# Kernel optimization log

Measured on AMD Instinct MI355X. Metric: run time of the kernel, lower is better.

Reference implementation:

```python
import jax, jax.numpy as jnp
import numpy as np

N = 50000      # nodes
E = 800000     # edges (avg degree 16)
DIM = 128      # in_dim == out_dim
H = 8          # num_heads
D = DIM // H   # per-head dim = 16


def layer_norm(x, g, b, eps=1e-5):
    m = x.mean(-1, keepdims=True)
    v = ((x - m) ** 2).mean(-1, keepdims=True)
    return (x - m) / jnp.sqrt(v + eps) * g + b


def setup_inputs() -> dict:
    key = jax.random.key(0)
    ks = jax.random.split(key, 16)
    w = 0.02
    return {
        "x": jax.random.normal(ks[0], (N, DIM), dtype=jnp.float32),
        "src": jax.random.randint(ks[1], (E,), 0, N),
        "dst": jax.random.randint(ks[2], (E,), 0, N),
        "Wq": jax.random.normal(ks[3], (DIM, DIM), dtype=jnp.float32) * w,
        "bq": jnp.zeros((DIM,), dtype=jnp.float32),
        "Wk": jax.random.normal(ks[4], (DIM, DIM), dtype=jnp.float32) * w,
        "bk": jnp.zeros((DIM,), dtype=jnp.float32),
        "Wv": jax.random.normal(ks[5], (DIM, DIM), dtype=jnp.float32) * w,
        "bv": jnp.zeros((DIM,), dtype=jnp.float32),
        "Wo": jax.random.normal(ks[6], (DIM, DIM), dtype=jnp.float32) * w,
        "bo": jnp.zeros((DIM,), dtype=jnp.float32),
        "ln1_g": jnp.ones((DIM,), dtype=jnp.float32),
        "ln1_b": jnp.zeros((DIM,), dtype=jnp.float32),
        "ln2_g": jnp.ones((DIM,), dtype=jnp.float32),
        "ln2_b": jnp.zeros((DIM,), dtype=jnp.float32),
    }


def reference(x, src, dst, Wq, bq, Wk, bk, Wv, bv, Wo, bo, ln1_g, ln1_b, ln2_g, ln2_b):
    # Q/K/V projections, split into heads: [N, H, D]
    Q = (x @ Wq + bq).reshape(N, H, D)
    K = (x @ Wk + bk).reshape(N, H, D)
    V = (x @ Wv + bv).reshape(N, H, D)

    # per-edge src_dot_dst: (K[src] * Q[dst]).sum(-1) -> [E, H, 1]
    score = (K[src] * Q[dst]).sum(-1, keepdims=True)
    # scaled_exp with clamp(-5, 5)
    score = jnp.exp(jnp.clip(score / np.sqrt(D).astype(np.float32), -5.0, 5.0))

    # scatter-sum of V[src] * score into dst nodes -> wV [N, H, D]
    wV = jax.ops.segment_sum(V[src] * score, dst, num_segments=N)
    # (the original also computes z = segment_sum(score) but never uses it)

    # residual + LayerNorm
    h = x + wV.reshape(N, DIM)
    h = layer_norm(h, ln1_g, ln1_b)

    # sublayer wrapper: h + relu(O(norm(h)))  (dropout=0)
    h = h + jax.nn.relu(layer_norm(h, ln2_g, ln2_b) @ Wo + bo)
    return h
```

## Files before the change

### kernel.cpp

```cpp
#include <hip/hip_runtime.h>
#include <hip/hip_bf16.h>

#define N_NODES 50000
#define N_EDGES 800000
#define DIM     128
#define CAP     96
#define PREP_BLOCKS 258
#define QKV_BLOCKS  1563

typedef __attribute__((ext_vector_type(8))) short bf16x8;
typedef __attribute__((ext_vector_type(4))) float f32x4;
typedef __fp16 f16;
typedef __attribute__((ext_vector_type(2))) __fp16 f16x2;

__device__ __forceinline__ unsigned short f2bf(float f) {
    union { float f; unsigned u; } c; c.f = f;
    unsigned r = c.u + 0x7fffu + ((c.u >> 16) & 1u);
    return (unsigned short)(r >> 16);
}
__device__ __forceinline__ float bfhi(unsigned int u) {
    union { unsigned int u; float f; } c; c.u = u & 0xffff0000u; return c.f;
}
__device__ __forceinline__ float bflo(unsigned int u) {
    union { unsigned int u; float f; } c; c.u = u << 16; return c.f;
}
__device__ __forceinline__ float bfs(unsigned short s) {
    union { unsigned int u; float f; } c; c.u = (unsigned)s << 16; return c.f;
}
__device__ __forceinline__ void unpack8(uint4 w, float* f) {
    f[0] = bflo(w.x); f[1] = bfhi(w.x);
    f[2] = bflo(w.y); f[3] = bfhi(w.y);
    f[4] = bflo(w.z); f[5] = bfhi(w.z);
    f[6] = bflo(w.w); f[7] = bfhi(w.w);
}

__global__ __launch_bounds__(256) void prep_kernel(
    const float* __restrict__ Wq, const float* __restrict__ Wk,
    const float* __restrict__ Wv, const float* __restrict__ Wo,
    const float* __restrict__ bq, const float* __restrict__ bk,
    const float* __restrict__ bv,
    unsigned short* __restrict__ WT, unsigned short* __restrict__ WoT,
    float* __restrict__ bqkv, int* __restrict__ counts)
{
    const int t = blockIdx.x * 256 + threadIdx.x;
    if (t < N_NODES) counts[(unsigned)t << 4] = 0;
    if (t < 384 * 128) {
        int j = t >> 7, k = t & 127;
        int which = j >> 7, jj = j & 127;
        const float* W = which == 0 ? Wq : which == 1 ? Wk : Wv;
        WT[t] = f2bf(W[k * 128 + jj]);
    } else if (t < 384 * 128 + 128 * 128) {
        int t2 = t - 384 * 128;
        int j = t2 >> 7, k = t2 & 127;
        WoT[t2] = f2bf(Wo[k * 128 + j]);
    } else if (t < 384 * 128 + 128 * 128 + 384) {
        int j = t - (384 * 128 + 128 * 128);
        bqkv[j] = j < 128 ? bq[j] : j < 256 ? bk[j - 128] : bv[j - 256];
    }
}

__global__ __launch_bounds__(256) void qkv_fill_kernel(
    const float* __restrict__ x, const unsigned short* __restrict__ WT,
    const float* __restrict__ bqkv,
    const int* __restrict__ src, const int* __restrict__ dst,
    int* __restrict__ counts, unsigned short* __restrict__ bucket,
    unsigned short* __restrict__ Q, unsigned char* __restrict__ K8,
    unsigned short* __restrict__ Vh )
{
    __shared__ union {
        unsigned short xs[32][136];
        unsigned short cs[32][384];
    } sh;

    const int b = blockIdx.x;

    if (b & 1) {
        const int e0 = (b >> 1) * 512 + threadIdx.x;
        int s0 = 0, d0 = 0, s1 = 0, d1 = 0;
        const bool v0 = e0 < N_EDGES;
        const bool v1 = e0 + 256 < N_EDGES;
        if (v0) { s0 = src[e0]; d0 = dst[e0]; }
        if (v1) { s1 = src[e0 + 256]; d1 = dst[e0 + 256]; }
        if (v0) {
            const int pos = atomicAdd(&counts[(unsigned)d0 << 4], 1);
            if (pos < CAP) bucket[(unsigned)d0 * CAP + pos] = (unsigned short)s0;
        }
        if (v1) {
            const int pos = atomicAdd(&counts[(unsigned)d1 << 4], 1);
            if (pos < CAP) bucket[(unsigned)d1 * CAP + pos] = (unsigned short)s1;
        }
        return;
    }

    const int w   = threadIdx.x >> 6;
    const int l   = threadIdx.x & 63;
    const int l15 = l & 15;
    const int lk  = l >> 4;
    const int n0  = (b >> 1) * 32;

    for (int idx = threadIdx.x; idx < 32 * 32; idx += 256) {
        const int row = idx >> 5, c4 = idx & 31;
        const int node = n0 + row;
        unsigned short s0 = 0, s1 = 0, s2 = 0, s3 = 0;
        if (node < N_NODES) {
            float4 f = ((const float4*)(x + (size_t)node * 128))[c4];
            s0 = f2bf(f.x); s1 = f2bf(f.y); s2 = f2bf(f.z); s3 = f2bf(f.w);
        }
        unsigned short* p = &sh.xs[row][c4 * 4];
        p[0] = s0; p[1] = s1; p[2] = s2; p[3] = s3;
    }
    __syncthreads();

    f32x4 acc[6][2];
#pragma unroll
    for (int t = 0; t < 6; ++t)
#pragma unroll
        for (int rg = 0; rg < 2; ++rg) acc[t][rg] = (f32x4){0.f, 0.f, 0.f, 0.f};

#pragma unroll
    for (int kk = 0; kk < 4; ++kk) {
        const int kb = kk * 32 + lk * 8;
        bf16x8 a[2];
#pragma unroll
        for (int rg = 0; rg < 2; ++rg)
            a[rg] = *(const bf16x8*)(&sh.xs[rg * 16 + l15][kb]);
#pragma unroll
        for (int t = 0; t < 6; ++t) {
            const int j0 = w * 96 + t * 16;
            bf16x8 bb = *(const bf16x8*)(WT + (size_t)(j0 + l15) * 128 + kb);
            acc[t][0] = __builtin_amdgcn_mfma_f32_16x16x32_bf16(a[0], bb, acc[t][0], 0, 0, 0);
            acc[t][1] = __builtin_amdgcn_mfma_f32_16x16x32_bf16(a[1], bb, acc[t][1], 0, 0, 0);
        }
    }
    __syncthreads();

#pragma unroll
    for (int t = 0; t < 6; ++t) {
        const int j = w * 96 + t * 16 + l15;
        const float bias = bqkv[j];
#pragma unroll
        for (int rg = 0; rg < 2; ++rg)
#pragma unroll
            for (int r = 0; r < 4; ++r)
                sh.cs[rg * 16 + lk * 4 + r][j] = f2bf(acc[t][rg][r] + bias);
    }
    __syncthreads();

    for (int idx = threadIdx.x; idx < 32 * 16; idx += 256) {
        const int row = idx >> 4, c8 = idx & 15;
        const int node = n0 + row;
        if (node < N_NODES)
            *(uint4*)(Q + (size_t)node * 128 + c8 * 8) =
                ((const uint4*)&sh.cs[row][0])[c8];
    }
    for (int idx = threadIdx.x; idx < 32 * 16; idx += 256) {
        const int row = idx >> 4, c8 = idx & 15;
        const int node = n0 + row;
        if (node < N_NODES) {
            const unsigned short* p = &sh.cs[row][128 + c8 * 8];
            int w0 = __builtin_amdgcn_cvt_pk_fp8_f32(bfs(p[0]), bfs(p[1]), 0, false);
            w0     = __builtin_amdgcn_cvt_pk_fp8_f32(bfs(p[2]), bfs(p[3]), w0, true);
            int w1 = __builtin_amdgcn_cvt_pk_fp8_f32(bfs(p[4]), bfs(p[5]), 0, false);
            w1     = __builtin_amdgcn_cvt_pk_fp8_f32(bfs(p[6]), bfs(p[7]), w1, true);
            *(uint2*)(K8 + (size_t)node * 128 + c8 * 8) =
                make_uint2((unsigned)w0, (unsigned)w1);
        }
    }
    for (int idx = threadIdx.x; idx < 32 * 16; idx += 256) {
        const int row = idx >> 4, c8 = idx & 15;
        const int node = n0 + row;
        if (node < N_NODES) {
            const unsigned short* p = &sh.cs[row][256 + c8 * 8];
            union { uint4 u; f16x2 h[4]; } vv;
            vv.h[0] = __builtin_amdgcn_cvt_pkrtz(bfs(p[0]), bfs(p[1]));
            vv.h[1] = __builtin_amdgcn_cvt_pkrtz(bfs(p[2]), bfs(p[3]));
            vv.h[2] = __builtin_amdgcn_cvt_pkrtz(bfs(p[4]), bfs(p[5]));
            vv.h[3] = __builtin_amdgcn_cvt_pkrtz(bfs(p[6]), bfs(p[7]));
            *(uint4*)(Vh + (size_t)node * 128 + c8 * 8) = vv.u;
        }
    }
}

__device__ __forceinline__ void edge_accum(uint2 kw, uint4 vw,
                                           const float* q, f16x2* acc2)
{
    float kf[8];
#if __has_builtin(__builtin_amdgcn_cvt_pk_f32_fp8)
    {
        auto p0 = __builtin_amdgcn_cvt_pk_f32_fp8((int)kw.x, false);
        auto p1 = __builtin_amdgcn_cvt_pk_f32_fp8((int)kw.x, true);
        auto p2 = __builtin_amdgcn_cvt_pk_f32_fp8((int)kw.y, false);
        auto p3 = __builtin_amdgcn_cvt_pk_f32_fp8((int)kw.y, true);
        kf[0] = p0[0]; kf[1] = p0[1]; kf[2] = p1[0]; kf[3] = p1[1];
        kf[4] = p2[0]; kf[5] = p2[1]; kf[6] = p3[0]; kf[7] = p3[1];
    }
#else
    kf[0] = __builtin_amdgcn_cvt_f32_fp8(kw.x, 0);
    kf[1] = __builtin_amdgcn_cvt_f32_fp8(kw.x, 1);
    kf[2] = __builtin_amdgcn_cvt_f32_fp8(kw.x, 2);
    kf[3] = __builtin_amdgcn_cvt_f32_fp8(kw.x, 3);
    kf[4] = __builtin_amdgcn_cvt_f32_fp8(kw.y, 0);
    kf[5] = __builtin_amdgcn_cvt_f32_fp8(kw.y, 1);
    kf[6] = __builtin_amdgcn_cvt_f32_fp8(kw.y, 2);
    kf[7] = __builtin_amdgcn_cvt_f32_fp8(kw.y, 3);
#endif
    float dot = q[0]*kf[0] + q[1]*kf[1] + q[2]*kf[2] + q[3]*kf[3]
              + q[4]*kf[4] + q[5]*kf[5] + q[6]*kf[6] + q[7]*kf[7];
    dot += __shfl_xor(dot, 1);
    float z = fminf(fmaxf(dot * 0.25f, -5.f), 5.f);
    float sc = __expf(z);
    f16x2 sc2 = __builtin_amdgcn_cvt_pkrtz(sc, sc);
    union { uint4 u; f16x2 h[4]; } v; v.u = vw;
#pragma unroll
    for (int j = 0; j < 4; ++j)
        acc2[j] = __builtin_elementwise_fma(v.h[j], sc2, acc2[j]);
}

__global__ __launch_bounds__(256) void gather_ln_kernel(
    const float* __restrict__ x,
    const unsigned short* __restrict__ Qb, const unsigned char* __restrict__ K8,
    const unsigned short* __restrict__ Vh,
    const int* __restrict__ counts, const unsigned short* __restrict__ bucket,
    const float* __restrict__ g1, const float* __restrict__ b1,
    unsigned short* __restrict__ h )
{
    const int node = blockIdx.x * 4 + (threadIdx.x >> 6);
    if (node >= N_NODES) return;
    const unsigned lane = threadIdx.x & 15;
    const unsigned grp  = (threadIdx.x >> 4) & 3;

    const uint4* Q4 = (const uint4*)Qb;
    const uint2* K2 = (const uint2*)K8;
    const uint4* V4 = (const uint4*)Vh;

    const float4* x4 = (const float4*)(x + (size_t)node * DIM);
    const float4 xa = x4[lane * 2], xb = x4[lane * 2 + 1];

    float q[8];
    unpack8(Q4[(unsigned)node * 16u + lane], q);

    int cnt = counts[(unsigned)node << 4];
    if (cnt > CAP) cnt = CAP;
    const unsigned base = (unsigned)node * CAP;

    f16x2 acc2[4];
#pragma unroll
    for (int j = 0; j < 4; ++j) acc2[j] = (f16x2){(f16)0.f, (f16)0.f};

    int i = grp;
    for (; i + 4 < cnt; i += 8) {
        const unsigned s0 = bucket[base + i];
        const unsigned s1 = bucket[base + i + 4];
        const uint2 kw0 = K2[s0 * 16u + lane];
        const uint4 vw0 = V4[s0 * 16u + lane];
        const uint2 kw1 = K2[s1 * 16u + lane];
        const uint4 vw1 = V4[s1 * 16u + lane];
        edge_accum(kw0, vw0, q, acc2);
        edge_accum(kw1, vw1, q, acc2);
    }
    if (i < cnt) {
        const unsigned s0 = bucket[base + i];
        const uint2 kw0 = K2[s0 * 16u + lane];
        const uint4 vw0 = V4[s0 * 16u + lane];
        edge_accum(kw0, vw0, q, acc2);
    }

#pragma unroll
    for (int j = 0; j < 4; ++j) {
        float t = __builtin_bit_cast(float, acc2[j]);
        t = __shfl_xor(t, 16);
        acc2[j] += __builtin_bit_cast(f16x2, t);
        t = __builtin_bit_cast(float, acc2[j]);
        t = __shfl_xor(t, 32);
        acc2[j] += __builtin_bit_cast(f16x2, t);
    }
    float wv[8];
#pragma unroll
    for (int j = 0; j < 4; ++j) {
        wv[2 * j]     = (float)acc2[j][0];
        wv[2 * j + 1] = (float)acc2[j][1];
    }

    float a[8] = { xa.x + wv[0], xa.y + wv[1], xa.z + wv[2], xa.w + wv[3],
                   xb.x + wv[4], xb.y + wv[5], xb.z + wv[6], xb.w + wv[7] };

    float sum = 0.f;
#pragma unroll
    for (int j = 0; j < 8; ++j) sum += a[j];
#pragma unroll
    for (int m = 1; m < 16; m <<= 1) sum += __shfl_xor(sum, m);
    float mean = sum * (1.f / 128.f);
    float vs = 0.f;
#pragma unroll
    for (int j = 0; j < 8; ++j) { a[j] -= mean; vs += a[j] * a[j]; }
#pragma unroll
    for (int m = 1; m < 16; m <<= 1) vs += __shfl_xor(vs, m);
    float rstd = rsqrtf(vs * (1.f / 128.f) + 1e-5f);

    if ((threadIdx.x & 63) < 16) {
        const float4 g1a = ((const float4*)g1)[lane * 2], g1b = ((const float4*)g1)[lane * 2 + 1];
        const float4 b1a = ((const float4*)b1)[lane * 2], b1b = ((const float4*)b1)[lane * 2 + 1];
        float hv[8];
        hv[0] = a[0] * rstd * g1a.x + b1a.x;  hv[1] = a[1] * rstd * g1a.y + b1a.y;
        hv[2] = a[2] * rstd * g1a.z + b1a.z;  hv[3] = a[3] * rstd * g1a.w + b1a.w;
        hv[4] = a[4] * rstd * g1b.x + b1b.x;  hv[5] = a[5] * rstd * g1b.y + b1b.y;
        hv[6] = a[6] * rstd * g1b.z + b1b.z;  hv[7] = a[7] * rstd * g1b.w + b1b.w;

        uint4 up;
        up.x = (unsigned)f2bf(hv[0]) | ((unsigned)f2bf(hv[1]) << 16);
        up.y = (unsigned)f2bf(hv[2]) | ((unsigned)f2bf(hv[3]) << 16);
        up.z = (unsigned)f2bf(hv[4]) | ((unsigned)f2bf(hv[5]) << 16);
        up.w = (unsigned)f2bf(hv[6]) | ((unsigned)f2bf(hv[7]) << 16);
        ((uint4*)(h + (size_t)node * DIM))[lane] = up;
    }
}

__global__ __launch_bounds__(256) void out_mfma(
    const unsigned short* __restrict__ h, const unsigned short* __restrict__ WoT,
    const float* __restrict__ g2, const float* __restrict__ b2,
    const float* __restrict__ bo, float* __restrict__ out)
{
    __shared__ unsigned short hs[32][136];
    __shared__ union {
        unsigned short us[32][136];
        float ls[32][128];
    } shB;

    const int w   = threadIdx.x >> 6;
    const int l   = threadIdx.x & 63;
    const int l15 = l & 15;
    const int lk  = l >> 4;
    const int n0  = blockIdx.x * 32;

    for (int idx = threadIdx.x; idx < 32 * 16; idx += 256) {
        const int row = idx >> 4, c8 = idx & 15;
        const int node = n0 + row;
        uint4 v = make_uint4(0, 0, 0, 0);
        if (node < N_NODES)
            v = ((const uint4*)(h + (size_t)node * 128))[c8];
        *(uint4*)(&hs[row][c8 * 8]) = v;
    }
    __syncthreads();

    {
        const int row = threadIdx.x >> 3;
        const int sub = threadIdx.x & 7;
        float v[16];
#pragma unroll
        for (int j = 0; j < 16; ++j) v[j] = bfs(hs[row][sub * 16 + j]);
        float sum = 0.f;
#pragma unroll
        for (int j = 0; j < 16; ++j) sum += v[j];
#pragma unroll
        for (int m = 1; m < 8; m <<= 1) sum += __shfl_xor(sum, m);
        float mean = sum * (1.f / 128.f);
        float vs = 0.f;
#pragma unroll
        for (int j = 0; j < 16; ++j) { v[j] -= mean; vs += v[j] * v[j]; }
#pragma unroll
        for (int m = 1; m < 8; m <<= 1) vs += __shfl_xor(vs, m);
        float rstd = rsqrtf(vs * (1.f / 128.f) + 1e-5f);
#pragma unroll
        for (int j4 = 0; j4 < 4; ++j4) {
            const float4 gg = ((const float4*)g2)[sub * 4 + j4];
            const float4 bb = ((const float4*)b2)[sub * 4 + j4];
            shB.us[row][sub * 16 + j4 * 4 + 0] = f2bf(v[j4 * 4 + 0] * rstd * gg.x + bb.x);
            shB.us[row][sub * 16 + j4 * 4 + 1] = f2bf(v[j4 * 4 + 1] * rstd * gg.y + bb.y);
            shB.us[row][sub * 16 + j4 * 4 + 2] = f2bf(v[j4 * 4 + 2] * rstd * gg.z + bb.z);
            shB.us[row][sub * 16 + j4 * 4 + 3] = f2bf(v[j4 * 4 + 3] * rstd * gg.w + bb.w);
        }
    }
    __syncthreads();

    f32x4 acc[2][2];
#pragma unroll
    for (int t = 0; t < 2; ++t)
#pragma unroll
        for (int rg = 0; rg < 2; ++rg) acc[t][rg] = (f32x4){0.f, 0.f, 0.f, 0.f};

#pragma unroll
    for (int kk = 0; kk < 4; ++kk) {
        const int kb = kk * 32 + lk * 8;
        bf16x8 a[2];
#pragma unroll
        for (int rg = 0; rg < 2; ++rg)
            a[rg] = *(const bf16x8*)(&shB.us[rg * 16 + l15][kb]);
#pragma unroll
        for (int t = 0; t < 2; ++t) {
            const int j0 = w * 32 + t * 16;
            bf16x8 b = *(const bf16x8*)(WoT + (size_t)(j0 + l15) * 128 + kb);
            acc[t][0] = __builtin_amdgcn_mfma_f32_16x16x32_bf16(a[0], b, acc[t][0], 0, 0, 0);
            acc[t][1] = __builtin_amdgcn_mfma_f32_16x16x32_bf16(a[1], b, acc[t][1], 0, 0, 0);
        }
    }
    __syncthreads();

#pragma unroll
    for (int t = 0; t < 2; ++t) {
        const int j = w * 32 + t * 16 + l15;
        const float bias = bo[j];
#pragma unroll
        for (int rg = 0; rg < 2; ++rg)
#pragma unroll
            for (int r = 0; r < 4; ++r)
                shB.ls[rg * 16 + lk * 4 + r][j] = fmaxf(acc[t][rg][r] + bias, 0.f);
    }
    __syncthreads();

    for (int idx = threadIdx.x; idx < 32 * 32; idx += 256) {
        const int row = idx >> 5, c4 = idx & 31;
        const int node = n0 + row;
        if (node < N_NODES) {
            float4 v = ((const float4*)shB.ls[row])[c4];
            const unsigned short* hp = &hs[row][c4 * 4];
            ((float4*)(out + (size_t)node * 128))[c4] = make_float4(
                bfs(hp[0]) + v.x, bfs(hp[1]) + v.y,
                bfs(hp[2]) + v.z, bfs(hp[3]) + v.w);
        }
    }
}

extern "C" void kernel_launch(void* const* d_in, const int* in_sizes, int n_in,
                              void* d_out, int out_size, void* d_ws, size_t ws_size,
                              hipStream_t stream)
{
    const float* x    = (const float*)d_in[0];
    const int*   src  = (const int*)  d_in[1];
    const int*   dst  = (const int*)  d_in[2];
    const float* Wq   = (const float*)d_in[3];
    const float* bq   = (const float*)d_in[4];
    const float* Wk   = (const float*)d_in[5];
    const float* bk   = (const float*)d_in[6];
    const float* Wv   = (const float*)d_in[7];
    const float* bv   = (const float*)d_in[8];
    const float* Wo   = (const float*)d_in[9];
    const float* bo   = (const float*)d_in[10];
    const float* ln1g = (const float*)d_in[11];
    const float* ln1b = (const float*)d_in[12];
    const float* ln2g = (const float*)d_in[13];
    const float* ln2b = (const float*)d_in[14];

    float* out = (float*)d_out;
    char*  wsb = (char*)d_ws;

    const size_t NM = (size_t)N_NODES * DIM;
    unsigned short* Qb = (unsigned short*)(wsb);
    unsigned short* Vh = Qb + NM;
    unsigned short* hb = Vh + NM;
    unsigned char*  K8 = (unsigned char*)(hb + NM);
    unsigned short* WT  = (unsigned short*)(K8 + NM);
    unsigned short* WoT = WT + 384 * 128;
    float* bqkv   = (float*)(WoT + 128 * 128);
    int*   counts = (int*)(bqkv + 384);
    unsigned short* bucket = (unsigned short*)(counts + (size_t)N_NODES * 16);

    prep_kernel<<<PREP_BLOCKS, 256, 0, stream>>>(
        Wq, Wk, Wv, Wo, bq, bk, bv, WT, WoT, bqkv, counts);

    qkv_fill_kernel<<<2 * QKV_BLOCKS, 256, 0, stream>>>(
        x, WT, bqkv, src, dst, counts, bucket, Qb, K8, Vh);

    gather_ln_kernel<<<(N_NODES + 3) / 4, 256, 0, stream>>>(
        x, Qb, K8, Vh, counts, bucket, ln1g, ln1b, hb);

    out_mfma<<<(N_NODES + 31) / 32, 256, 0, stream>>>(
        hb, WoT, ln2g, ln2b, bo, out);
}
```

Measured before the change: 124.9 us.

## Fuse edge bucketing into QKV blocks and preload bucket ids via wave shuffle

The QKV kernel no longer alternates between edge-bucketing blocks and GEMM blocks. Every block now issues its edge atomics first, runs the projection GEMM, and writes the bucket entries at the end, so atomic latency overlaps with the matrix work and the grid is half as large. In the gather kernel, each wave loads up to 64 bucket source ids in one coalesced read and broadcasts them with shuffles instead of doing a dependent scalar load per edge. Invalid edges are masked by zeroing their score, which lets the loop run with a uniform trip count but wastes some loads on padded slots.

```diff
diff --git a/kernel.cpp b/kernel.cpp
--- a/kernel.cpp
+++ b/kernel.cpp
@@ -72,42 +72,32 @@
         unsigned short cs[32][384];
     } sh;
 
-    const int b = blockIdx.x;
-
-    if (b & 1) {
-        const int e0 = (b >> 1) * 512 + threadIdx.x;
-        int s0 = 0, d0 = 0, s1 = 0, d1 = 0;
-        const bool v0 = e0 < N_EDGES;
-        const bool v1 = e0 + 256 < N_EDGES;
-        if (v0) { s0 = src[e0]; d0 = dst[e0]; }
-        if (v1) { s1 = src[e0 + 256]; d1 = dst[e0 + 256]; }
-        if (v0) {
-            const int pos = atomicAdd(&counts[(unsigned)d0 << 4], 1);
-            if (pos < CAP) bucket[(unsigned)d0 * CAP + pos] = (unsigned short)s0;
-        }
-        if (v1) {
-            const int pos = atomicAdd(&counts[(unsigned)d1 << 4], 1);
-            if (pos < CAP) bucket[(unsigned)d1 * CAP + pos] = (unsigned short)s1;
-        }
-        return;
-    }
+    const int e0 = blockIdx.x * 512 + threadIdx.x;
+    const int e1 = e0 + 256;
+    const bool v0 = e0 < N_EDGES;
+    const bool v1 = e1 < N_EDGES;
+    int s0 = 0, d0 = 0, s1 = 0, d1 = 0, pos0 = CAP, pos1 = CAP;
+    if (v0) { s0 = src[e0]; d0 = dst[e0]; }
+    if (v1) { s1 = src[e1]; d1 = dst[e1]; }
+    if (v0) pos0 = atomicAdd(&counts[(unsigned)d0 << 4], 1);
+    if (v1) pos1 = atomicAdd(&counts[(unsigned)d1 << 4], 1);
 
     const int w   = threadIdx.x >> 6;
     const int l   = threadIdx.x & 63;
     const int l15 = l & 15;
     const int lk  = l >> 4;
-    const int n0  = (b >> 1) * 32;
+    const int n0  = blockIdx.x * 32;
 
     for (int idx = threadIdx.x; idx < 32 * 32; idx += 256) {
         const int row = idx >> 5, c4 = idx & 31;
         const int node = n0 + row;
-        unsigned short s0 = 0, s1 = 0, s2 = 0, s3 = 0;
+        unsigned short t0 = 0, t1 = 0, t2 = 0, t3 = 0;
         if (node < N_NODES) {
             float4 f = ((const float4*)(x + (size_t)node * 128))[c4];
-            s0 = f2bf(f.x); s1 = f2bf(f.y); s2 = f2bf(f.z); s3 = f2bf(f.w);
+            t0 = f2bf(f.x); t1 = f2bf(f.y); t2 = f2bf(f.z); t3 = f2bf(f.w);
         }
         unsigned short* p = &sh.xs[row][c4 * 4];
-        p[0] = s0; p[1] = s1; p[2] = s2; p[3] = s3;
+        p[0] = t0; p[1] = t1; p[2] = t2; p[3] = t3;
     }
     __syncthreads();
 
@@ -179,10 +169,14 @@
             *(uint4*)(Vh + (size_t)node * 128 + c8 * 8) = vv.u;
         }
     }
+
+    if (v0 && pos0 < CAP) bucket[(unsigned)d0 * CAP + pos0] = (unsigned short)s0;
+    if (v1 && pos1 < CAP) bucket[(unsigned)d1 * CAP + pos1] = (unsigned short)s1;
 }
 
 __device__ __forceinline__ void edge_accum(uint2 kw, uint4 vw,
-                                           const float* q, f16x2* acc2)
+                                           const float* q, f16x2* acc2,
+                                           bool val)
 {
     float kf[8];
 #if __has_builtin(__builtin_amdgcn_cvt_pk_f32_fp8)
@@ -209,6 +203,7 @@
     dot += __shfl_xor(dot, 1);
     float z = fminf(fmaxf(dot * 0.25f, -5.f), 5.f);
     float sc = __expf(z);
+    sc = val ? sc : 0.f;
     f16x2 sc2 = __builtin_amdgcn_cvt_pkrtz(sc, sc);
     union { uint4 u; f16x2 h[4]; } v; v.u = vw;
 #pragma unroll
@@ -226,8 +221,9 @@
 {
     const int node = blockIdx.x * 4 + (threadIdx.x >> 6);
     if (node >= N_NODES) return;
-    const unsigned lane = threadIdx.x & 15;
-    const unsigned grp  = (threadIdx.x >> 4) & 3;
+    const unsigned lane  = threadIdx.x & 15;
+    const unsigned grp   = (threadIdx.x >> 4) & 3;
+    const int      lane64 = threadIdx.x & 63;
 
     const uint4* Q4 = (const uint4*)Qb;
     const uint2* K2 = (const uint2*)K8;
@@ -243,26 +239,42 @@
     if (cnt > CAP) cnt = CAP;
     const unsigned base = (unsigned)node * CAP;
 
+    int pid = 0;
+    if (lane64 < cnt) pid = bucket[base + lane64];
+
     f16x2 acc2[4];
 #pragma unroll
     for (int j = 0; j < 4; ++j) acc2[j] = (f16x2){(f16)0.f, (f16)0.f};
 
-    int i = grp;
-    for (; i + 4 < cnt; i += 8) {
-        const unsigned s0 = bucket[base + i];
-        const unsigned s1 = bucket[base + i + 4];
+    const int kmax = (cnt + 3) >> 2;
+    int k = 0;
+    for (; k + 2 <= kmax; k += 2) {
+        const int ia = 4 * k + grp;
+        const int ib = ia + 4;
+        const bool va = ia < cnt;
+        const bool vb = ib < cnt;
+        const int ial = va ? ia : 0;
+        const int ibl = vb ? ib : 0;
+        const unsigned s0 = (ial < 64) ? (unsigned)__shfl(pid, ial, 64)
+                                       : (unsigned)bucket[base + ial];
+        const unsigned s1 = (ibl < 64) ? (unsigned)__shfl(pid, ibl, 64)
+                                       : (unsigned)bucket[base + ibl];
         const uint2 kw0 = K2[s0 * 16u + lane];
         const uint4 vw0 = V4[s0 * 16u + lane];
         const uint2 kw1 = K2[s1 * 16u + lane];
         const uint4 vw1 = V4[s1 * 16u + lane];
-        edge_accum(kw0, vw0, q, acc2);
-        edge_accum(kw1, vw1, q, acc2);
-    }
-    if (i < cnt) {
-        const unsigned s0 = bucket[base + i];
+        edge_accum(kw0, vw0, q, acc2, va);
+        edge_accum(kw1, vw1, q, acc2, vb);
+    }
+    if (k < kmax) {
+        const int ia = 4 * k + grp;
+        const bool va = ia < cnt;
+        const int ial = va ? ia : 0;
+        const unsigned s0 = (ial < 64) ? (unsigned)__shfl(pid, ial, 64)
+                                       : (unsigned)bucket[base + ial];
         const uint2 kw0 = K2[s0 * 16u + lane];
         const uint4 vw0 = V4[s0 * 16u + lane];
-        edge_accum(kw0, vw0, q, acc2);
+        edge_accum(kw0, vw0, q, acc2, va);
     }
 
 #pragma unroll
@@ -297,7 +309,7 @@
     for (int m = 1; m < 16; m <<= 1) vs += __shfl_xor(vs, m);
     float rstd = rsqrtf(vs * (1.f / 128.f) + 1e-5f);
 
-    if ((threadIdx.x & 63) < 16) {
+    if (lane64 < 16) {
         const float4 g1a = ((const float4*)g1)[lane * 2], g1b = ((const float4*)g1)[lane * 2 + 1];
         const float4 b1a = ((const float4*)b1)[lane * 2], b1b = ((const float4*)b1)[lane * 2 + 1];
         float hv[8];
@@ -457,7 +469,7 @@
     prep_kernel<<<PREP_BLOCKS, 256, 0, stream>>>(
         Wq, Wk, Wv, Wo, bq, bk, bv, WT, WoT, bqkv, counts);
 
-    qkv_fill_kernel<<<2 * QKV_BLOCKS, 256, 0, stream>>>(
+    qkv_fill_kernel<<<QKV_BLOCKS, 256, 0, stream>>>(
         x, WT, bqkv, src, dst, counts, bucket, Qb, K8, Vh);
 
     gather_ln_kernel<<<(N_NODES + 3) / 4, 256, 0, stream>>>(
```

Result: slower. 136.6 us (+9.4%).
